# Performance work log

Hardware: AMD Instinct MI355X
Metric: run time of the kernel (lower is better)

The kernel has to match this reference:

```python
import jax, jax.numpy as jnp
import numpy as np

S = 16        # each mode size of the TT shape (16,16,16,16)
R = 4         # bond dimension
B = 1024      # batch
INIT_STD = 0.05  # keras 'random_normal' initializer stddev


def setup_inputs() -> dict:
    key = jax.random.key(0)
    ks = jax.random.split(key, 6)
    x = jax.random.normal(ks[0], (B, S * S * S * S), dtype=jnp.float32)
    # TT cores, per build(): core_1 (S,S,R); middle cores (S,S,R,R); last core (S,S,R)
    G1 = INIT_STD * jax.random.normal(ks[1], (S, S, R), dtype=jnp.float32)
    G2 = INIT_STD * jax.random.normal(ks[2], (S, S, R, R), dtype=jnp.float32)
    G3 = INIT_STD * jax.random.normal(ks[3], (S, S, R, R), dtype=jnp.float32)
    G4 = INIT_STD * jax.random.normal(ks[4], (S, S, R), dtype=jnp.float32)
    bias = jnp.zeros((S, S, S, S), dtype=jnp.float32)  # tf.zeros(shape=self.shape)
    return {"x": x, "G1": G1, "G2": G2, "G3": G3, "G4": G4, "bias": bias}


def reference(x, G1, G2, G3, G4, bias):
    # Per sample: reshape to (S,S,S,S) and contract the TT chain (ncon network):
    # out[a,b,c,d] = sum_{i,j,k,l,r,s,t} x[i,j,k,l] G1[a,i,r] G2[b,j,r,s] G3[c,k,s,t] G4[d,l,t]
    n = x.shape[0]
    xr = x.reshape(n, S, S, S, S)
    out = jnp.einsum('nijkl,air,bjrs,ckst,dlt->nabcd', xr, G1, G2, G3, G4,
                     optimize=True)
    out = out + bias  # broadcast bias over batch
    return jax.nn.relu(out.reshape(n, S * S * S * S))
```

## Files before the change

### kernel.cpp

```cpp
#include <hip/hip_runtime.h>
#include <hip/hip_bf16.h>


typedef __attribute__((ext_vector_type(8))) short bf16x8;
typedef __attribute__((ext_vector_type(4))) float f32x4;
typedef unsigned short u16;
typedef unsigned long long u64;

#define T2_PER_N 262144
#define PAD40 40
#define PAD72 72

static __device__ __forceinline__ u16 f2bf(float f) {
  __hip_bfloat16 h = __float2bfloat16(f);
  return *reinterpret_cast<u16*>(&h);
}
static __device__ __forceinline__ u64 pack4(f32x4 a) {
  union { u16 s[4]; u64 u; } p;
  p.s[0] = f2bf(a[0]); p.s[1] = f2bf(a[1]); p.s[2] = f2bf(a[2]); p.s[3] = f2bf(a[3]);
  return p.u;
}
#define MFMA(A, B, C) __builtin_amdgcn_mfma_f32_16x16x32_bf16((A), (B), (C), 0, 0, 0)

__global__ __launch_bounds__(256, 2) void tt_passA(
    const float* __restrict__ x, const float* __restrict__ G1,
    const float* __restrict__ G2, u16* __restrict__ T2, int n0)
{
  const int tid = threadIdx.x;
  const int k    = blockIdx.x;
  const int slot = blockIdx.y;
  const int n = n0 + slot;
  const int lane = tid & 63, w = tid >> 6, quad = lane >> 4, ln = lane & 15;

  __shared__ __align__(16) u16 xs [256 * PAD40];
  __shared__ __align__(16) u16 g1s[ 64 * PAD40];
  __shared__ __align__(16) u16 t1s[256 * PAD72];
  __shared__ __align__(16) u16 g2s[ 64 * PAD72];

  {
    const uint4 z = {0, 0, 0, 0};
    for (int idx = tid; idx < 640; idx += 256) {
      if (idx < 512) *(uint4*)&xs [(idx >> 1) * PAD40 + 16 + (idx & 1) * 8] = z;
      else           *(uint4*)&g1s[((idx - 512) >> 1) * PAD40 + 16 + (idx & 1) * 8] = z;
    }
  }
  #pragma unroll
  for (int it = 0; it < 4; ++it) {
    const int e = it * 256 + tid, a = e >> 6, i = (e >> 2) & 15, r = e & 3;
    g1s[(a * 4 + r) * PAD40 + i] = f2bf(G1[e]);
  }
  #pragma unroll
  for (int it = 0; it < 16; ++it) {
    const int e = it * 256 + tid, b = e >> 8, j = (e >> 4) & 15, r = (e >> 2) & 3, s = e & 3;
    g2s[(b * 4 + s) * PAD72 + j * 4 + r] = f2bf(G2[e]);
  }
  {
    const float4* xg = (const float4*)x + (size_t)n * 16384;
    #pragma unroll
    for (int it = 0; it < 4; ++it) {
      const int e = it * 256 + tid, i = (e >> 2) & 15, j = e >> 6, lq = e & 3;
      const float4 v = xg[i * 1024 + j * 64 + k * 4 + lq];
      const float vv[4] = {v.x, v.y, v.z, v.w};
      #pragma unroll
      for (int u = 0; u < 4; ++u) xs[(j * 16 + lq * 4 + u) * PAD40 + i] = f2bf(vv[u]);
    }
  }
  __syncthreads();

  {
    bf16x8 a1[4];
    #pragma unroll
    for (int t = 0; t < 4; ++t)
      a1[t] = *(const bf16x8*)&xs[((w * 4 + t) * 16 + ln) * PAD40 + quad * 8];
    #pragma unroll
    for (int tn = 0; tn < 4; ++tn) {
      const bf16x8 b1 = *(const bf16x8*)&g1s[(tn * 16 + ln) * PAD40 + quad * 8];
      #pragma unroll
      for (int t = 0; t < 4; ++t) {
        f32x4 acc = {0.f, 0.f, 0.f, 0.f};
        acc = MFMA(b1, a1[t], acc);
        *(u64*)&t1s[((tn * 4 + quad) * 16 + ln) * PAD72 + (w * 4 + t) * 4] = pack4(acc);
      }
    }
  }
  __syncthreads();

  {
    bf16x8 a2[4][2];
    #pragma unroll
    for (int t = 0; t < 4; ++t)
      #pragma unroll
      for (int ks = 0; ks < 2; ++ks)
        a2[t][ks] = *(const bf16x8*)&t1s[((w * 4 + t) * 16 + ln) * PAD72 + ks * 32 + quad * 8];
    __syncthreads();
    #pragma unroll
    for (int tn = 0; tn < 4; ++tn) {
      const bf16x8 b20 = *(const bf16x8*)&g2s[(tn * 16 + ln) * PAD72 + quad * 8];
      const bf16x8 b21 = *(const bf16x8*)&g2s[(tn * 16 + ln) * PAD72 + 32 + quad * 8];
      #pragma unroll
      for (int t = 0; t < 4; ++t) {
        f32x4 acc = {0.f, 0.f, 0.f, 0.f};
        acc = MFMA(b20, a2[t][0], acc);
        acc = MFMA(b21, a2[t][1], acc);
        *(u64*)&t1s[((w * 4 + t) * 16 + ln) * PAD72 + tn * 16 + quad * 4] = pack4(acc);
      }
    }
  }
  __syncthreads();

  {
    uint4* Tg = (uint4*)(T2 + (size_t)slot * T2_PER_N);
    #pragma unroll
    for (int it = 0; it < 8; ++it) {
      const int e = it * 256 + tid, row = e >> 3, seg = e & 7;
      const uint4 q = *(const uint4*)&t1s[row * PAD72 + seg * 8];
      Tg[(row >> 4) * 2048 + k * 128 + (row & 15) * 8 + seg] = q;
    }
  }
}

__global__ __launch_bounds__(256, 2) void tt_passB(
    const u16* __restrict__ T2, const float* __restrict__ G3,
    const float* __restrict__ G4, const float* __restrict__ bias,
    float* __restrict__ out, int n0)
{
  const int tid = threadIdx.x;
  const int a    = blockIdx.x;
  const int slot = blockIdx.y;
  const int n = n0 + slot;
  const int lane = tid & 63, w = tid >> 6, quad = lane >> 4, ln = lane & 15;

  __shared__ __align__(16) u16 t2a[256 * PAD72];
  __shared__ __align__(16) u16 g3s[ 64 * PAD72];
  __shared__ __align__(16) u16 g4s[ 16 * PAD72];

  #pragma unroll
  for (int it = 0; it < 16; ++it) {
    const int e = it * 256 + tid, c = e >> 8, k = (e >> 4) & 15, s = (e >> 2) & 3, t = e & 3;
    g3s[(c * 4 + t) * PAD72 + k * 4 + s] = f2bf(G3[e]);
  }
  #pragma unroll
  for (int it = 0; it < 4; ++it) {
    const int e = it * 256 + tid, d = e >> 6, l = (e >> 2) & 15, t = e & 3;
    g4s[d * PAD72 + t * 16 + l] = f2bf(G4[e]);
  }
  {
    const uint4* Tg = (const uint4*)(T2 + (size_t)slot * T2_PER_N) + a * 2048;
    #pragma unroll
    for (int it = 0; it < 8; ++it) {
      const int e = it * 256 + tid, kl = e >> 3, bq = e & 7;
      const uint4 q = Tg[e];
      const int k = kl >> 4, l = kl & 15, b0 = bq * 2;
      const u64 lo = ((u64)q.y << 32) | q.x, hi = ((u64)q.w << 32) | q.z;
      *(u64*)&t2a[(b0 * 16 + l) * PAD72 + k * 4]      = lo;
      *(u64*)&t2a[(b0 * 16 + l + 16) * PAD72 + k * 4] = hi;
    }
  }
  __syncthreads();

  {
    bf16x8 a3[4][2];
    #pragma unroll
    for (int t = 0; t < 4; ++t)
      #pragma unroll
      for (int ks = 0; ks < 2; ++ks)
        a3[t][ks] = *(const bf16x8*)&t2a[((w * 4 + t) * 16 + ln) * PAD72 + ks * 32 + quad * 8];
    __syncthreads();
    #pragma unroll
    for (int tn = 0; tn < 4; ++tn) {
      const bf16x8 b30 = *(const bf16x8*)&g3s[(tn * 16 + ln) * PAD72 + quad * 8];
      const bf16x8 b31 = *(const bf16x8*)&g3s[(tn * 16 + ln) * PAD72 + 32 + quad * 8];
      #pragma unroll
      for (int t = 0; t < 4; ++t) {
        f32x4 acc = {0.f, 0.f, 0.f, 0.f};
        acc = MFMA(a3[t][0], b30, acc);
        acc = MFMA(a3[t][1], b31, acc);
        *(u64*)&t2a[((w * 4 + t) * 16 + tn * 4 + (ln >> 2)) * PAD72 + (ln & 3) * 16 + quad * 4]
            = pack4(acc);
      }
    }
  }
  __syncthreads();

  {
    bf16x8 b4[2];
    #pragma unroll
    for (int ks = 0; ks < 2; ++ks)
      b4[ks] = *(const bf16x8*)&g4s[ln * PAD72 + ks * 32 + quad * 8];
    const size_t obase = (size_t)n * 65536;
    #pragma unroll
    for (int t = 0; t < 4; ++t) {
      bf16x8 a40 = *(const bf16x8*)&t2a[((w * 4 + t) * 16 + ln) * PAD72 + quad * 8];
      bf16x8 a41 = *(const bf16x8*)&t2a[((w * 4 + t) * 16 + ln) * PAD72 + 32 + quad * 8];
      f32x4 acc = {0.f, 0.f, 0.f, 0.f};
      acc = MFMA(a40, b4[0], acc);
      acc = MFMA(a41, b4[1], acc);
      #pragma unroll
      for (int r = 0; r < 4; ++r) {
        const int m4 = (w * 4 + t) * 16 + quad * 4 + r;
        const int off = a * 4096 + m4 * 16 + ln;
        const float v = acc[r] + bias[off];
        out[obase + off] = fmaxf(v, 0.f);
      }
    }
  }
}

extern "C" void kernel_launch(void* const* d_in, const int* in_sizes, int n_in,
                              void* d_out, int out_size, void* d_ws, size_t ws_size,
                              hipStream_t stream) {
  const float* x    = (const float*)d_in[0];
  const float* G1   = (const float*)d_in[1];
  const float* G2   = (const float*)d_in[2];
  const float* G3   = (const float*)d_in[3];
  const float* G4   = (const float*)d_in[4];
  const float* bias = (const float*)d_in[5];
  float* out = (float*)d_out;
  u16* T2 = (u16*)d_ws;

  const int B = 1024;
  const size_t per_n = (size_t)T2_PER_N * sizeof(u16);
  int chunk = (int)(ws_size / per_n);
  if (chunk > B) chunk = B;
  if (chunk < 1) chunk = 1;

  for (int nn0 = 0; nn0 < B; nn0 += chunk) {
    const int c = (nn0 + chunk <= B) ? chunk : (B - nn0);
    tt_passA<<<dim3(16, c), 256, 0, stream>>>(x, G1, G2, T2, nn0);
    tt_passB<<<dim3(16, c), 256, 0, stream>>>(T2, G3, G4, bias, out, nn0);
  }
}
```

Measured before the change: 667.6 us.

## Precompute bf16 core images once, widen blocks to 512 threads, cap chunk size

A one-block prep kernel converts G1..G4 to padded bf16 layouts in workspace once, so passA and passB copy ready-made images into shared memory instead of converting per block. Both passes move to 512-thread blocks with two tiles per wave, and passA handles two k slices per block, reusing the staged G1/G2 image. The batch chunk is capped at 256 samples to keep the T2 intermediate smaller and more likely to stay in cache. The risks are more chunk iterations and kernel launches, plus extra barriers in passA's k loop.

```diff
diff --git a/kernel.cpp b/kernel.cpp
--- a/kernel.cpp
+++ b/kernel.cpp
@@ -11,6 +11,7 @@
 #define PAD40 40
 #define PAD72 72
 
+
 static __device__ __forceinline__ u16 f2bf(float f) {
   __hip_bfloat16 h = __float2bfloat16(f);
   return *reinterpret_cast<u16*>(&h);
@@ -22,160 +23,173 @@
 }
 #define MFMA(A, B, C) __builtin_amdgcn_mfma_f32_16x16x32_bf16((A), (B), (C), 0, 0, 0)
 
-__global__ __launch_bounds__(256, 2) void tt_passA(
-    const float* __restrict__ x, const float* __restrict__ G1,
-    const float* __restrict__ G2, u16* __restrict__ T2, int n0)
+__global__ void tt_prep(const float* __restrict__ G1, const float* __restrict__ G2,
+                        const float* __restrict__ G3, const float* __restrict__ G4,
+                        u16* __restrict__ img)
 {
   const int tid = threadIdx.x;
-  const int k    = blockIdx.x;
+  const uint4 z = {0, 0, 0, 0};
+  for (int idx = tid; idx < 1616; idx += 256) ((uint4*)img)[idx] = z;
+  __syncthreads();
+  #pragma unroll
+  for (int it = 0; it < 4; ++it) {
+    const int e = it * 256 + tid, a = e >> 6, i = (e >> 2) & 15, r = e & 3;
+    img[(a * 4 + r) * PAD40 + i] = f2bf(G1[e]);
+  }
+  #pragma unroll
+  for (int it = 0; it < 16; ++it) {
+    const int e = it * 256 + tid, b = e >> 8, j = (e >> 4) & 15, r = (e >> 2) & 3, s = e & 3;
+    img[2560 + (b * 4 + s) * PAD72 + j * 4 + r] = f2bf(G2[e]);
+  }
+  #pragma unroll
+  for (int it = 0; it < 16; ++it) {
+    const int e = it * 256 + tid, c = e >> 8, k = (e >> 4) & 15, s = (e >> 2) & 3, t = e & 3;
+    img[7168 + (c * 4 + t) * PAD72 + k * 4 + s] = f2bf(G3[e]);
+  }
+  #pragma unroll
+  for (int it = 0; it < 4; ++it) {
+    const int e = it * 256 + tid, d = e >> 6, l = (e >> 2) & 15, t = e & 3;
+    img[11776 + d * PAD72 + t * 16 + l] = f2bf(G4[e]);
+  }
+}
+
+__global__ __launch_bounds__(512, 4) void tt_passA(
+    const float* __restrict__ x, const u16* __restrict__ img,
+    u16* __restrict__ T2, int n0)
+{
+  const int tid = threadIdx.x;
+  const int kp   = blockIdx.x;
   const int slot = blockIdx.y;
   const int n = n0 + slot;
-  const int lane = tid & 63, w = tid >> 6, quad = lane >> 4, ln = lane & 15;
-
+  const int lane = tid & 63, w = tid >> 6, quad = (lane >> 4) & 3, ln = lane & 15;
+
+  __shared__ __align__(16) u16 gAs[7168];
   __shared__ __align__(16) u16 xs [256 * PAD40];
-  __shared__ __align__(16) u16 g1s[ 64 * PAD40];
   __shared__ __align__(16) u16 t1s[256 * PAD72];
-  __shared__ __align__(16) u16 g2s[ 64 * PAD72];
-
+
+  for (int idx = tid; idx < 896; idx += 512)
+    ((uint4*)gAs)[idx] = ((const uint4*)img)[idx];
   {
     const uint4 z = {0, 0, 0, 0};
-    for (int idx = tid; idx < 640; idx += 256) {
-      if (idx < 512) *(uint4*)&xs [(idx >> 1) * PAD40 + 16 + (idx & 1) * 8] = z;
-      else           *(uint4*)&g1s[((idx - 512) >> 1) * PAD40 + 16 + (idx & 1) * 8] = z;
-    }
-  }
-  #pragma unroll
-  for (int it = 0; it < 4; ++it) {
-    const int e = it * 256 + tid, a = e >> 6, i = (e >> 2) & 15, r = e & 3;
-    g1s[(a * 4 + r) * PAD40 + i] = f2bf(G1[e]);
-  }
-  #pragma unroll
-  for (int it = 0; it < 16; ++it) {
-    const int e = it * 256 + tid, b = e >> 8, j = (e >> 4) & 15, r = (e >> 2) & 3, s = e & 3;
-    g2s[(b * 4 + s) * PAD72 + j * 4 + r] = f2bf(G2[e]);
-  }
-  {
-    const float4* xg = (const float4*)x + (size_t)n * 16384;
+    const int row = tid >> 1, h = tid & 1;
+    *(uint4*)&xs[row * PAD40 + 16 + h * 8] = z;
+  }
+
+  const float4* xg = (const float4*)x + (size_t)n * 16384;
+  uint4* Tg = (uint4*)(T2 + (size_t)slot * T2_PER_N);
+
+  #pragma unroll
+  for (int kx = 0; kx < 2; ++kx) {
+    const int k = kp * 2 + kx;
+    #pragma unroll
+    for (int it = 0; it < 2; ++it) {
+      const int e = it * 512 + tid, i = (e >> 2) & 15, j = e >> 6, lq = e & 3;
+      const float4 v = xg[i * 1024 + j * 64 + k * 4 + lq];
+      xs[(j * 16 + lq * 4 + 0) * PAD40 + i] = f2bf(v.x);
+      xs[(j * 16 + lq * 4 + 1) * PAD40 + i] = f2bf(v.y);
+      xs[(j * 16 + lq * 4 + 2) * PAD40 + i] = f2bf(v.z);
+      xs[(j * 16 + lq * 4 + 3) * PAD40 + i] = f2bf(v.w);
+    }
+    __syncthreads();
+
+    {
+      bf16x8 a1[2];
+      #pragma unroll
+      for (int t = 0; t < 2; ++t)
+        a1[t] = *(const bf16x8*)&xs[((w * 2 + t) * 16 + ln) * PAD40 + quad * 8];
+      #pragma unroll
+      for (int tn = 0; tn < 4; ++tn) {
+        const bf16x8 b1 = *(const bf16x8*)&gAs[(tn * 16 + ln) * PAD40 + quad * 8];
+        #pragma unroll
+        for (int t = 0; t < 2; ++t) {
+          f32x4 acc = {0.f, 0.f, 0.f, 0.f};
+          acc = MFMA(b1, a1[t], acc);
+          *(u64*)&t1s[((tn * 4 + quad) * 16 + ln) * PAD72 + (w * 2 + t) * 4] = pack4(acc);
+        }
+      }
+    }
+    __syncthreads();
+
+    {
+      bf16x8 a2[2][2];
+      #pragma unroll
+      for (int t = 0; t < 2; ++t)
+        #pragma unroll
+        for (int ks = 0; ks < 2; ++ks)
+          a2[t][ks] = *(const bf16x8*)&t1s[((w * 2 + t) * 16 + ln) * PAD72 + ks * 32 + quad * 8];
+      __syncthreads();
+      const u16* g2s = gAs + 2560;
+      #pragma unroll
+      for (int tn = 0; tn < 4; ++tn) {
+        const bf16x8 b20 = *(const bf16x8*)&g2s[(tn * 16 + ln) * PAD72 + quad * 8];
+        const bf16x8 b21 = *(const bf16x8*)&g2s[(tn * 16 + ln) * PAD72 + 32 + quad * 8];
+        #pragma unroll
+        for (int t = 0; t < 2; ++t) {
+          f32x4 acc = {0.f, 0.f, 0.f, 0.f};
+          acc = MFMA(b20, a2[t][0], acc);
+          acc = MFMA(b21, a2[t][1], acc);
+          *(u64*)&t1s[((w * 2 + t) * 16 + ln) * PAD72 + tn * 16 + quad * 4] = pack4(acc);
+        }
+      }
+    }
+    __syncthreads();
+
     #pragma unroll
     for (int it = 0; it < 4; ++it) {
-      const int e = it * 256 + tid, i = (e >> 2) & 15, j = e >> 6, lq = e & 3;
-      const float4 v = xg[i * 1024 + j * 64 + k * 4 + lq];
-      const float vv[4] = {v.x, v.y, v.z, v.w};
-      #pragma unroll
-      for (int u = 0; u < 4; ++u) xs[(j * 16 + lq * 4 + u) * PAD40 + i] = f2bf(vv[u]);
-    }
-  }
-  __syncthreads();
-
-  {
-    bf16x8 a1[4];
-    #pragma unroll
-    for (int t = 0; t < 4; ++t)
-      a1[t] = *(const bf16x8*)&xs[((w * 4 + t) * 16 + ln) * PAD40 + quad * 8];
-    #pragma unroll
-    for (int tn = 0; tn < 4; ++tn) {
-      const bf16x8 b1 = *(const bf16x8*)&g1s[(tn * 16 + ln) * PAD40 + quad * 8];
-      #pragma unroll
-      for (int t = 0; t < 4; ++t) {
-        f32x4 acc = {0.f, 0.f, 0.f, 0.f};
-        acc = MFMA(b1, a1[t], acc);
-        *(u64*)&t1s[((tn * 4 + quad) * 16 + ln) * PAD72 + (w * 4 + t) * 4] = pack4(acc);
-      }
-    }
-  }
-  __syncthreads();
-
-  {
-    bf16x8 a2[4][2];
-    #pragma unroll
-    for (int t = 0; t < 4; ++t)
-      #pragma unroll
-      for (int ks = 0; ks < 2; ++ks)
-        a2[t][ks] = *(const bf16x8*)&t1s[((w * 4 + t) * 16 + ln) * PAD72 + ks * 32 + quad * 8];
-    __syncthreads();
-    #pragma unroll
-    for (int tn = 0; tn < 4; ++tn) {
-      const bf16x8 b20 = *(const bf16x8*)&g2s[(tn * 16 + ln) * PAD72 + quad * 8];
-      const bf16x8 b21 = *(const bf16x8*)&g2s[(tn * 16 + ln) * PAD72 + 32 + quad * 8];
-      #pragma unroll
-      for (int t = 0; t < 4; ++t) {
-        f32x4 acc = {0.f, 0.f, 0.f, 0.f};
-        acc = MFMA(b20, a2[t][0], acc);
-        acc = MFMA(b21, a2[t][1], acc);
-        *(u64*)&t1s[((w * 4 + t) * 16 + ln) * PAD72 + tn * 16 + quad * 4] = pack4(acc);
-      }
-    }
-  }
-  __syncthreads();
-
-  {
-    uint4* Tg = (uint4*)(T2 + (size_t)slot * T2_PER_N);
-    #pragma unroll
-    for (int it = 0; it < 8; ++it) {
-      const int e = it * 256 + tid, row = e >> 3, seg = e & 7;
+      const int e = it * 512 + tid, row = e >> 3, seg = e & 7;
       const uint4 q = *(const uint4*)&t1s[row * PAD72 + seg * 8];
       Tg[(row >> 4) * 2048 + k * 128 + (row & 15) * 8 + seg] = q;
     }
   }
 }
 
-__global__ __launch_bounds__(256, 2) void tt_passB(
-    const u16* __restrict__ T2, const float* __restrict__ G3,
-    const float* __restrict__ G4, const float* __restrict__ bias,
-    float* __restrict__ out, int n0)
+__global__ __launch_bounds__(512, 4) void tt_passB(
+    const u16* __restrict__ T2, const u16* __restrict__ img,
+    const float* __restrict__ bias, float* __restrict__ out, int n0)
 {
   const int tid = threadIdx.x;
   const int a    = blockIdx.x;
   const int slot = blockIdx.y;
   const int n = n0 + slot;
-  const int lane = tid & 63, w = tid >> 6, quad = lane >> 4, ln = lane & 15;
-
+  const int lane = tid & 63, w = tid >> 6, quad = (lane >> 4) & 3, ln = lane & 15;
+
+  __shared__ __align__(16) u16 gBs[5760];
   __shared__ __align__(16) u16 t2a[256 * PAD72];
-  __shared__ __align__(16) u16 g3s[ 64 * PAD72];
-  __shared__ __align__(16) u16 g4s[ 16 * PAD72];
-
-  #pragma unroll
-  for (int it = 0; it < 16; ++it) {
-    const int e = it * 256 + tid, c = e >> 8, k = (e >> 4) & 15, s = (e >> 2) & 3, t = e & 3;
-    g3s[(c * 4 + t) * PAD72 + k * 4 + s] = f2bf(G3[e]);
-  }
-  #pragma unroll
-  for (int it = 0; it < 4; ++it) {
-    const int e = it * 256 + tid, d = e >> 6, l = (e >> 2) & 15, t = e & 3;
-    g4s[d * PAD72 + t * 16 + l] = f2bf(G4[e]);
-  }
+
+  for (int idx = tid; idx < 720; idx += 512)
+    ((uint4*)gBs)[idx] = ((const uint4*)(img + 7168))[idx];
   {
     const uint4* Tg = (const uint4*)(T2 + (size_t)slot * T2_PER_N) + a * 2048;
     #pragma unroll
-    for (int it = 0; it < 8; ++it) {
-      const int e = it * 256 + tid, kl = e >> 3, bq = e & 7;
+    for (int it = 0; it < 4; ++it) {
+      const int e = it * 512 + tid, kl = e >> 3, bq = e & 7;
       const uint4 q = Tg[e];
       const int k = kl >> 4, l = kl & 15, b0 = bq * 2;
       const u64 lo = ((u64)q.y << 32) | q.x, hi = ((u64)q.w << 32) | q.z;
-      *(u64*)&t2a[(b0 * 16 + l) * PAD72 + k * 4]      = lo;
-      *(u64*)&t2a[(b0 * 16 + l + 16) * PAD72 + k * 4] = hi;
+      *(u64*)&t2a[(b0 * 16 + l) * PAD72 + k * 4]       = lo;
+      *(u64*)&t2a[((b0 + 1) * 16 + l) * PAD72 + k * 4] = hi;
     }
   }
   __syncthreads();
 
   {
-    bf16x8 a3[4][2];
-    #pragma unroll
-    for (int t = 0; t < 4; ++t)
+    bf16x8 a3[2][2];
+    #pragma unroll
+    for (int t = 0; t < 2; ++t)
       #pragma unroll
       for (int ks = 0; ks < 2; ++ks)
-        a3[t][ks] = *(const bf16x8*)&t2a[((w * 4 + t) * 16 + ln) * PAD72 + ks * 32 + quad * 8];
+        a3[t][ks] = *(const bf16x8*)&t2a[((w * 2 + t) * 16 + ln) * PAD72 + ks * 32 + quad * 8];
     __syncthreads();
     #pragma unroll
     for (int tn = 0; tn < 4; ++tn) {
-      const bf16x8 b30 = *(const bf16x8*)&g3s[(tn * 16 + ln) * PAD72 + quad * 8];
-      const bf16x8 b31 = *(const bf16x8*)&g3s[(tn * 16 + ln) * PAD72 + 32 + quad * 8];
-      #pragma unroll
-      for (int t = 0; t < 4; ++t) {
+      const bf16x8 b30 = *(const bf16x8*)&gBs[(tn * 16 + ln) * PAD72 + quad * 8];
+      const bf16x8 b31 = *(const bf16x8*)&gBs[(tn * 16 + ln) * PAD72 + 32 + quad * 8];
+      #pragma unroll
+      for (int t = 0; t < 2; ++t) {
         f32x4 acc = {0.f, 0.f, 0.f, 0.f};
         acc = MFMA(a3[t][0], b30, acc);
         acc = MFMA(a3[t][1], b31, acc);
-        *(u64*)&t2a[((w * 4 + t) * 16 + tn * 4 + (ln >> 2)) * PAD72 + (ln & 3) * 16 + quad * 4]
+        *(u64*)&t2a[((w * 2 + t) * 16 + tn * 4 + (ln >> 2)) * PAD72 + (ln & 3) * 16 + quad * 4]
             = pack4(acc);
       }
     }
@@ -183,21 +197,22 @@
   __syncthreads();
 
   {
+    const u16* g4s = gBs + 4608;
     bf16x8 b4[2];
     #pragma unroll
     for (int ks = 0; ks < 2; ++ks)
       b4[ks] = *(const bf16x8*)&g4s[ln * PAD72 + ks * 32 + quad * 8];
     const size_t obase = (size_t)n * 65536;
     #pragma unroll
-    for (int t = 0; t < 4; ++t) {
-      bf16x8 a40 = *(const bf16x8*)&t2a[((w * 4 + t) * 16 + ln) * PAD72 + quad * 8];
-      bf16x8 a41 = *(const bf16x8*)&t2a[((w * 4 + t) * 16 + ln) * PAD72 + 32 + quad * 8];
+    for (int t = 0; t < 2; ++t) {
+      bf16x8 a40 = *(const bf16x8*)&t2a[((w * 2 + t) * 16 + ln) * PAD72 + quad * 8];
+      bf16x8 a41 = *(const bf16x8*)&t2a[((w * 2 + t) * 16 + ln) * PAD72 + 32 + quad * 8];
       f32x4 acc = {0.f, 0.f, 0.f, 0.f};
       acc = MFMA(a40, b4[0], acc);
       acc = MFMA(a41, b4[1], acc);
       #pragma unroll
       for (int r = 0; r < 4; ++r) {
-        const int m4 = (w * 4 + t) * 16 + quad * 4 + r;
+        const int m4 = (w * 2 + t) * 16 + quad * 4 + r;
         const int off = a * 4096 + m4 * 16 + ln;
         const float v = acc[r] + bias[off];
         out[obase + off] = fmaxf(v, 0.f);
@@ -216,17 +231,20 @@
   const float* G4   = (const float*)d_in[4];
   const float* bias = (const float*)d_in[5];
   float* out = (float*)d_out;
-  u16* T2 = (u16*)d_ws;
-
-  const int B = 1024;
+  u16* img = (u16*)d_ws;
+  u16* T2  = (u16*)d_ws + 16384;
+
+  const int Bn = 1024;
   const size_t per_n = (size_t)T2_PER_N * sizeof(u16);
-  int chunk = (int)(ws_size / per_n);
-  if (chunk > B) chunk = B;
+  size_t avail = (ws_size > 32768) ? (ws_size - 32768) : 0;
+  int chunk = (int)(avail / per_n);
+  if (chunk > 256) chunk = 256;
   if (chunk < 1) chunk = 1;
 
-  for (int nn0 = 0; nn0 < B; nn0 += chunk) {
-    const int c = (nn0 + chunk <= B) ? chunk : (B - nn0);
-    tt_passA<<<dim3(16, c), 256, 0, stream>>>(x, G1, G2, T2, nn0);
-    tt_passB<<<dim3(16, c), 256, 0, stream>>>(T2, G3, G4, bias, out, nn0);
-  }
-}
+  tt_prep<<<1, 256, 0, stream>>>(G1, G2, G3, G4, img);
+  for (int nn0 = 0; nn0 < Bn; nn0 += chunk) {
+    const int c = (nn0 + chunk <= Bn) ? chunk : (Bn - nn0);
+    tt_passA<<<dim3(8, c), 512, 0, stream>>>(x, img, T2, nn0);
+    tt_passB<<<dim3(16, c), 512, 0, stream>>>(T2, img, bias, out, nn0);
+  }
+}
```

Result: faster. 639.0 us (-4.3%).
